# Kernel tuning notes

Measured on AMD Instinct MI355X. Metric: run time of the kernel, lower is better.

## Reference

```python
import jax, jax.numpy as jnp
import numpy as np

N_NODES = 100000
N_EDGES = 1600000
IN_DIM = 64
HID_DIM = 64
OUT_DIM = 1


def setup_inputs() -> dict:
    key = jax.random.key(0)
    ks = jax.random.split(key, 5)
    x = jax.random.normal(ks[0], (N_NODES, IN_DIM), dtype=jnp.float32)
    edge_index = jax.random.randint(ks[1], (2, N_EDGES), 0, N_NODES, dtype=jnp.int64)
    s1 = 1.0 / np.sqrt(IN_DIM)
    s2 = 1.0 / np.sqrt(HID_DIM)
    W1 = jax.random.normal(ks[2], (IN_DIM, HID_DIM), dtype=jnp.float32) * s1
    b1 = jnp.zeros((HID_DIM,), dtype=jnp.float32)
    W2 = jax.random.normal(ks[3], (HID_DIM, HID_DIM), dtype=jnp.float32) * s2
    b2 = jnp.zeros((HID_DIM,), dtype=jnp.float32)
    Wp = jax.random.normal(ks[4], (HID_DIM, OUT_DIM), dtype=jnp.float32) * s2
    bp = jnp.zeros((OUT_DIM,), dtype=jnp.float32)
    return {"x": x, "edge_index": edge_index, "W1": W1, "b1": b1,
            "W2": W2, "b2": b2, "Wp": Wp, "bp": bp}


def _gcn_conv(x, src, dst, deg_inv_sqrt, W, b):
    # PyG GCNConv: linear transform, then deg-normalized scatter-add aggregation
    h = x @ W  # [N, out]
    norm = deg_inv_sqrt[src] * deg_inv_sqrt[dst]  # [E_total]
    msg = h[src] * norm[:, None]  # gather + scale, [E_total, out]
    agg = jax.ops.segment_sum(msg, dst, num_segments=x.shape[0])
    return agg + b


def reference(x, edge_index, W1, b1, W2, b2, Wp, bp):
    n = x.shape[0]
    # add self-loops (as PyG GCNConv does by default)
    loop = jnp.arange(n, dtype=edge_index.dtype)
    src = jnp.concatenate([edge_index[0], loop])
    dst = jnp.concatenate([edge_index[1], loop])
    # symmetric normalization from in-degree over dst (includes self-loops)
    deg = jax.ops.segment_sum(jnp.ones_like(dst, dtype=x.dtype), dst, num_segments=n)
    deg_inv_sqrt = jnp.where(deg > 0, jax.lax.rsqrt(jnp.maximum(deg, 1e-12)), 0.0)
    h = jax.nn.relu(_gcn_conv(x, src, dst, deg_inv_sqrt, W1, b1))
    # dropout(p=0.3) is identity at eval time
    h = jax.nn.relu(_gcn_conv(h, src, dst, deg_inv_sqrt, W2, b2))
    return h @ Wp + bp  # [N, OUT_DIM]
```

## Files before the change

kernel.cpp:

```cpp
#include <hip/hip_runtime.h>
#include <hip/hip_fp16.h>


#define GNN_N 100000
#define GNN_E 1600000
#define NBUCK 391
#define HBLK  500
#define EPBH  3200
#define NBLK  250
#define EPB   6400
#define SCTILE 16
#define STAGE_CAP 4864
#define DUMMY_OFF (GNN_N * 128)

typedef _Float16 half8 __attribute__((ext_vector_type(8)));
typedef float f32x4 __attribute__((ext_vector_type(4)));

__global__ __launch_bounds__(256) void k_hist(const int* __restrict__ dst,
                                              int* __restrict__ hist,
                                              __half* __restrict__ TA,
                                              __half* __restrict__ TB) {
    __shared__ int h[NBUCK];
    for (int i = threadIdx.x; i < NBUCK; i += 256) h[i] = 0;
    if (blockIdx.x == 0 && threadIdx.x < 16) {
        uint4 z = {0, 0, 0, 0};
        int t = threadIdx.x;
        __half* base = (t < 8) ? TA : TB;
        *(uint4*)((char*)base + DUMMY_OFF + (t & 7) * 16) = z;
    }
    __syncthreads();
    int b = blockIdx.x;
    int e0 = b * EPBH, e1 = min(e0 + EPBH, GNN_E);
    for (int e = e0 + threadIdx.x * 4; e < e1; e += 1024) {
        int4 d = *(const int4*)(dst + e);
        atomicAdd(&h[d.x >> 8], 1);
        atomicAdd(&h[d.y >> 8], 1);
        atomicAdd(&h[d.z >> 8], 1);
        atomicAdd(&h[d.w >> 8], 1);
    }
    __syncthreads();
    for (int i = threadIdx.x; i < NBUCK; i += 256)
        hist[b * NBUCK + i] = h[i];
}

__global__ __launch_bounds__(256) void k_cscan(int* __restrict__ hist,
                                               int* __restrict__ tot) {
    __shared__ int tile[256][SCTILE + 1];
    int k0 = blockIdx.x * SCTILE;
    int b = threadIdx.x;
    int lane = b & 63, w = b >> 6;
    int cSub = lane >> 4;
    int l16 = lane & 15;
    int col = w * 4 + cSub;
    int run = 0;
    for (int pass = 0; pass < 2; ++pass) {
        int r = pass * 256 + b;
#pragma unroll
        for (int i = 0; i < SCTILE; ++i) {
            int k = k0 + i;
            tile[b][i] = (k < NBUCK && r < HBLK) ? hist[r * NBUCK + k] : 0;
        }
        __syncthreads();
        for (int chunk = 0; chunk < 16; ++chunk) {
            int idx = chunk * 16 + l16;
            int v = tile[idx][col];
            int s = v;
#pragma unroll
            for (int o = 1; o < 16; o <<= 1) {
                int t = __shfl_up(s, o);
                if (l16 >= o) s += t;
            }
            tile[idx][col] = s - v + run;
            run += __shfl(s, lane | 15);
        }
        __syncthreads();
#pragma unroll
        for (int i = 0; i < SCTILE; ++i) {
            int k = k0 + i;
            if (k < NBUCK && r < HBLK) hist[r * NBUCK + k] = tile[b][i];
        }
        __syncthreads();
    }
    if (l16 == 0 && k0 + col < NBUCK) tot[k0 + col] = run;
}

__global__ __launch_bounds__(512) void k_btot(const int* __restrict__ tot,
                                              int* __restrict__ bbase,
                                              int* __restrict__ cbase) {
    __shared__ int s[512];
    int t = threadIdx.x;
    int own = (t < NBUCK) ? tot[t] : 0;
    s[t] = own;
    __syncthreads();
    for (int off = 1; off < 512; off <<= 1) {
        int v = (t >= off) ? s[t - off] : 0;
        __syncthreads();
        s[t] += v;
        __syncthreads();
    }
    if (t < NBUCK) {
        int ex = s[t] - own;
        bbase[t] = ex;
        cbase[t] = (ex & ~3) + t * 772;
    }
    if (t == 0) bbase[NBUCK] = GNN_E;
}

__global__ __launch_bounds__(256) void k_part(const int* __restrict__ src,
                                              const int* __restrict__ dst,
                                              const int* __restrict__ hist,
                                              const int* __restrict__ bbase,
                                              unsigned int* __restrict__ part) {
    __shared__ int off[NBUCK];
    int b = blockIdx.x;
    for (int i = threadIdx.x; i < NBUCK; i += 256)
        off[i] = bbase[i] + hist[(2 * b) * NBUCK + i];
    __syncthreads();
    int e0 = b * EPB, e1 = min(e0 + EPB, GNN_E);
    for (int e = e0 + threadIdx.x * 4; e < e1; e += 1024) {
        int4 d = *(const int4*)(dst + e);
        int4 s = *(const int4*)(src + e);
        int sl0 = atomicAdd(&off[d.x >> 8], 1);
        part[sl0] = ((unsigned int)(d.x & 255) << 17) | (unsigned int)s.x;
        int sl1 = atomicAdd(&off[d.y >> 8], 1);
        part[sl1] = ((unsigned int)(d.y & 255) << 17) | (unsigned int)s.y;
        int sl2 = atomicAdd(&off[d.z >> 8], 1);
        part[sl2] = ((unsigned int)(d.z & 255) << 17) | (unsigned int)s.z;
        int sl3 = atomicAdd(&off[d.w >> 8], 1);
        part[sl3] = ((unsigned int)(d.w & 255) << 17) | (unsigned int)s.w;
    }
}

__global__ __launch_bounds__(256) void k_bsort(const unsigned int* __restrict__ part,
                                               const int* __restrict__ bbase,
                                               const int* __restrict__ cbase,
                                               int* __restrict__ csr,
                                               int* __restrict__ rowptr,
                                               int* __restrict__ deg,
                                               float* __restrict__ dis) {
    __shared__ int cnt[256];
    __shared__ int pstart[256];
    __shared__ int bump[256];
    __shared__ int wtot[4];
    __shared__ unsigned int stage[STAGE_CAP];
    int k = blockIdx.x;
    int t = threadIdx.x;
    cnt[t] = 0;
    __syncthreads();
    int e0 = bbase[k], e1 = bbase[k + 1];
    int m = e1 - e0;
    bool fits = (m <= STAGE_CAP);
    for (int i = t; i < m; i += 256) {
        unsigned int p = part[e0 + i];
        if (fits) stage[i] = p;
        atomicAdd(&cnt[p >> 17], 1);
    }
    __syncthreads();
    int c = cnt[t];
    int padded = (c + 3) & ~3;
    int v = padded;
#pragma unroll
    for (int o = 1; o < 64; o <<= 1) {
        int u = __shfl_up(v, o);
        if ((t & 63) >= o) v += u;
    }
    if ((t & 63) == 63) wtot[t >> 6] = v;
    __syncthreads();
    int wb = 0;
#pragma unroll
    for (int j = 0; j < 4; ++j)
        if (j < (t >> 6)) wb += wtot[j];
    pstart[t] = wb + v - padded;
    bump[t] = pstart[t];
    __syncthreads();
    int cb = cbase[k];
    int node = k * 256 + t;
    if (node < GNN_N) {
        rowptr[node] = cb + pstart[t];
        deg[node]    = padded;
        dis[node]    = rsqrtf((float)c + 1.0f);
    }
    for (int i = t; i < m; i += 256) {
        unsigned int p = fits ? stage[i] : part[e0 + i];
        int slot = atomicAdd(&bump[p >> 17], 1);
        csr[cb + slot] = (int)(p & 0x1FFFF) << 7;
    }
    __syncthreads();
    if (node < GNN_N) {
        for (int i = c; i < padded; ++i)
            csr[cb + pstart[t] + i] = DUMMY_OFF;
    }
}

template<typename TIN>
__global__ __launch_bounds__(256) void k_mmf(const TIN* __restrict__ X,
                                             const float* __restrict__ W,
                                             const float* __restrict__ dis,
                                             __half* __restrict__ Y, int n) {
    __shared__ __align__(16) __half Xs[64][72];
    __shared__ __align__(16) __half Wt[64][72];
    __shared__ float disS[64];
    int tid = threadIdx.x;
    int base = blockIdx.x * 64;
    for (int i = tid; i < 4096; i += 256) {
        int k = i >> 6, j = i & 63;
        Wt[j][k] = __float2half(W[i]);
    }
    if (tid < 64) disS[tid] = (base + tid < n) ? dis[base + tid] : 0.f;
    if constexpr (sizeof(TIN) == 4) {
#pragma unroll
        for (int ii = 0; ii < 4; ++ii) {
            int i = ii * 256 + tid;
            int r = i >> 4, c4 = i & 15;
            int row = base + r;
            float4 vv = (row < n) ? ((const float4*)(X + (size_t)row * 64))[c4]
                                  : make_float4(0.f, 0.f, 0.f, 0.f);
            *(__half2*)&Xs[r][c4 * 4 + 0] = __floats2half2_rn(vv.x, vv.y);
            *(__half2*)&Xs[r][c4 * 4 + 2] = __floats2half2_rn(vv.z, vv.w);
        }
    } else {
#pragma unroll
        for (int ii = 0; ii < 2; ++ii) {
            int i = ii * 256 + tid;
            int r = i >> 3, c8 = i & 7;
            int row = base + r;
            uint4 u = {0, 0, 0, 0};
            if (row < n)
                u = *(const uint4*)((const __half*)X + (size_t)row * 64 + c8 * 8);
            *(uint4*)&Xs[r][c8 * 8] = u;
        }
    }
    __syncthreads();
    int w = tid >> 6, lane = tid & 63;
    int ar = w * 16 + (lane & 15);
    int ak = (lane >> 4) * 8;
    half8 a0 = *(const half8*)&Xs[ar][ak];
    half8 a1 = *(const half8*)&Xs[ar][32 + ak];
    f32x4 acc0 = {0.f, 0.f, 0.f, 0.f}, acc1 = acc0, acc2 = acc0, acc3 = acc0;
#define MMCOL(ACC, C) {                                                   \
        half8 b0 = *(const half8*)&Wt[(C) * 16 + (lane & 15)][ak];        \
        half8 b1 = *(const half8*)&Wt[(C) * 16 + (lane & 15)][32 + ak];   \
        ACC = __builtin_amdgcn_mfma_f32_16x16x32_f16(a0, b0, ACC, 0, 0, 0); \
        ACC = __builtin_amdgcn_mfma_f32_16x16x32_f16(a1, b1, ACC, 0, 0, 0); }
    MMCOL(acc0, 0) MMCOL(acc1, 1) MMCOL(acc2, 2) MMCOL(acc3, 3)
#undef MMCOL
    __syncthreads();
#define DST(ACC, C) {                                                     \
        _Pragma("unroll")                                                 \
        for (int i = 0; i < 4; ++i) {                                     \
            int rl = w * 16 + (lane >> 4) * 4 + i;                        \
            Xs[rl][(C) * 16 + (lane & 15)] = __float2half(ACC[i] * disS[rl]); \
        } }
    DST(acc0, 0) DST(acc1, 1) DST(acc2, 2) DST(acc3, 3)
#undef DST
    __syncthreads();
#pragma unroll
    for (int ii = 0; ii < 2; ++ii) {
        int i = ii * 256 + tid;
        int r = i >> 3, c8 = i & 7;
        int row = base + r;
        if (row < n)
            *(uint4*)(Y + (size_t)row * 64 + c8 * 8) = *(const uint4*)&Xs[r][c8 * 8];
    }
}

#define ACC8(A, U) {                                                     \
    float2 f_;                                                           \
    f_ = __half22float2(*(__half2*)&U.x); A[0] += f_.x; A[1] += f_.y;    \
    f_ = __half22float2(*(__half2*)&U.y); A[2] += f_.x; A[3] += f_.y;    \
    f_ = __half22float2(*(__half2*)&U.z); A[4] += f_.x; A[5] += f_.y;    \
    f_ = __half22float2(*(__half2*)&U.w); A[6] += f_.x; A[7] += f_.y; }

template<bool HEAD>
__global__ __launch_bounds__(256) void k_gatherg(
        const __half* __restrict__ T, const int* __restrict__ csr,
        const int* __restrict__ rowptr, const int* __restrict__ deg,
        const float* __restrict__ dis, const float* __restrict__ bias,
        const float* __restrict__ Wp, const float* __restrict__ bp,
        void* __restrict__ outv, int n) {
    int tid = threadIdx.x;
    int q = tid & 7;
    int node = blockIdx.x * 32 + (tid >> 3);
    if (node >= n) return;
    int base = rowptr[node];
    int cnt  = deg[node];
    float dd = dis[node];
    const char* Tq = (const char*)T + q * 16;
    float a0[8], a1[8];
#pragma unroll
    for (int i = 0; i < 8; ++i) { a0[i] = 0.f; a1[i] = 0.f; }
    int j = 0;
    for (; j + 8 <= cnt; j += 8) {
        int4 c0 = *(const int4*)(csr + base + j);
        int4 c1 = *(const int4*)(csr + base + j + 4);
        uint4 u0 = *(const uint4*)(Tq + (size_t)(unsigned)c0.x);
        uint4 u1 = *(const uint4*)(Tq + (size_t)(unsigned)c0.y);
        uint4 u2 = *(const uint4*)(Tq + (size_t)(unsigned)c0.z);
        uint4 u3 = *(const uint4*)(Tq + (size_t)(unsigned)c0.w);
        uint4 u4 = *(const uint4*)(Tq + (size_t)(unsigned)c1.x);
        uint4 u5 = *(const uint4*)(Tq + (size_t)(unsigned)c1.y);
        uint4 u6 = *(const uint4*)(Tq + (size_t)(unsigned)c1.z);
        uint4 u7 = *(const uint4*)(Tq + (size_t)(unsigned)c1.w);
        ACC8(a0, u0) ACC8(a1, u1) ACC8(a0, u2) ACC8(a1, u3)
        ACC8(a0, u4) ACC8(a1, u5) ACC8(a0, u6) ACC8(a1, u7)
    }
    if (j < cnt) {
        int4 c0 = *(const int4*)(csr + base + j);
        uint4 u0 = *(const uint4*)(Tq + (size_t)(unsigned)c0.x);
        uint4 u1 = *(const uint4*)(Tq + (size_t)(unsigned)c0.y);
        uint4 u2 = *(const uint4*)(Tq + (size_t)(unsigned)c0.z);
        uint4 u3 = *(const uint4*)(Tq + (size_t)(unsigned)c0.w);
        ACC8(a0, u0) ACC8(a1, u1) ACC8(a0, u2) ACC8(a1, u3)
    }
    uint4 us = *(const uint4*)(Tq + (size_t)node * 128);
    ACC8(a1, us)
    float4 bb0 = ((const float4*)bias)[q * 2 + 0];
    float4 bb1 = ((const float4*)bias)[q * 2 + 1];
    float r[8];
    r[0] = fmaxf(dd * (a0[0] + a1[0]) + bb0.x, 0.f);
    r[1] = fmaxf(dd * (a0[1] + a1[1]) + bb0.y, 0.f);
    r[2] = fmaxf(dd * (a0[2] + a1[2]) + bb0.z, 0.f);
    r[3] = fmaxf(dd * (a0[3] + a1[3]) + bb0.w, 0.f);
    r[4] = fmaxf(dd * (a0[4] + a1[4]) + bb1.x, 0.f);
    r[5] = fmaxf(dd * (a0[5] + a1[5]) + bb1.y, 0.f);
    r[6] = fmaxf(dd * (a0[6] + a1[6]) + bb1.z, 0.f);
    r[7] = fmaxf(dd * (a0[7] + a1[7]) + bb1.w, 0.f);
    if constexpr (HEAD) {
        float4 w0 = ((const float4*)Wp)[q * 2 + 0];
        float4 w1 = ((const float4*)Wp)[q * 2 + 1];
        float s = r[0] * w0.x + r[1] * w0.y + r[2] * w0.z + r[3] * w0.w
                + r[4] * w1.x + r[5] * w1.y + r[6] * w1.z + r[7] * w1.w;
#pragma unroll
        for (int m = 1; m <= 4; m <<= 1) s += __shfl_xor(s, m);
        if (q == 0) ((float*)outv)[node] = s + bp[0];
    } else {
        __half* op = (__half*)outv + (size_t)node * 64 + q * 8;
        uint4 u;
        *(__half2*)&u.x = __floats2half2_rn(r[0], r[1]);
        *(__half2*)&u.y = __floats2half2_rn(r[2], r[3]);
        *(__half2*)&u.z = __floats2half2_rn(r[4], r[5]);
        *(__half2*)&u.w = __floats2half2_rn(r[6], r[7]);
        *(uint4*)op = u;
    }
}

extern "C" void kernel_launch(void* const* d_in, const int* in_sizes, int n_in,
                              void* d_out, int out_size, void* d_ws, size_t ws_size,
                              hipStream_t stream) {
    const float* x  = (const float*)d_in[0];
    const int*   ei = (const int*)d_in[1];
    const float* W1 = (const float*)d_in[2];
    const float* b1 = (const float*)d_in[3];
    const float* W2 = (const float*)d_in[4];
    const float* b2 = (const float*)d_in[5];
    const float* Wp = (const float*)d_in[6];
    const float* bp = (const float*)d_in[7];
    float* out = (float*)d_out;

    const int N = GNN_N, E = GNN_E;
    const int* srcv = ei;
    const int* dstv = ei + E;

    char* ws = (char*)d_ws;
    int*    hist   = (int*)(ws + 0);
    int*    bbase  = (int*)(ws + 784000);
    int*    cbase  = (int*)(ws + 785600);
    int*    rowptr = (int*)(ws + 787200);
    int*    deg    = (int*)(ws + 1187200);
    float*  dis    = (float*)(ws + 1587200);
    int*    tot    = (int*)(ws + 1587200);
    int*    csr    = (int*)(ws + 1987200);
    __half* TA     = (__half*)(ws + 9597440);
    __half* h1h    = (__half*)(ws + 22410368);
    __half* TB     = (__half*)(ws + 35210368);
    unsigned int* part = (unsigned int*)(ws + 48023296);

    k_hist <<<HBLK, 256, 0, stream>>>(dstv, hist, TA, TB);
    k_cscan<<<(NBUCK + SCTILE - 1) / SCTILE, 256, 0, stream>>>(hist, tot);
    k_btot <<<1, 512, 0, stream>>>(tot, bbase, cbase);
    k_part <<<NBLK, 256, 0, stream>>>(srcv, dstv, hist, bbase, part);
    k_bsort<<<NBUCK, 256, 0, stream>>>(part, bbase, cbase, csr, rowptr, deg, dis);

    k_mmf<float><<<(N + 63) / 64, 256, 0, stream>>>(x, W1, dis, TA, N);
    k_gatherg<false><<<(N + 31) / 32, 256, 0, stream>>>(TA, csr, rowptr, deg, dis,
                                                        b1, nullptr, nullptr, h1h, N);
    k_mmf<__half><<<(N + 63) / 64, 256, 0, stream>>>(h1h, W2, dis, TB, N);
    k_gatherg<true><<<(N + 31) / 32, 256, 0, stream>>>(TB, csr, rowptr, deg, dis,
                                                       b2, Wp, bp, out, N);
}
```

Baseline: 132.0 us.

## Fuse layer-1 aggregation with layer-2 linear transform via in-block MFMA

The first-layer gather kernel now stages its 32 aggregated, ReLU'd rows in shared memory and multiplies them by W2 with MFMA, scaling by deg_inv_sqrt and writing the layer-2 transformed features directly. This removes a separate matmul launch and the write-then-read round trip of the intermediate hidden tensor through global memory. In exchange, each gather block converts W2 into shared memory, uses more LDS and adds barriers, which may lower occupancy of the latency-bound gather. The launch assumes N is divisible by 32.

After: 127.5 us. 1.04x faster.

```diff
diff --git a/kernel.cpp b/kernel.cpp
--- a/kernel.cpp
+++ b/kernel.cpp
@@ -192,8 +192,7 @@
     }
 }
 
-template<typename TIN>
-__global__ __launch_bounds__(256) void k_mmf(const TIN* __restrict__ X,
+__global__ __launch_bounds__(256) void k_mmf(const float* __restrict__ X,
                                              const float* __restrict__ W,
                                              const float* __restrict__ dis,
                                              __half* __restrict__ Y, int n) {
@@ -207,28 +206,15 @@
         Wt[j][k] = __float2half(W[i]);
     }
     if (tid < 64) disS[tid] = (base + tid < n) ? dis[base + tid] : 0.f;
-    if constexpr (sizeof(TIN) == 4) {
-#pragma unroll
-        for (int ii = 0; ii < 4; ++ii) {
-            int i = ii * 256 + tid;
-            int r = i >> 4, c4 = i & 15;
-            int row = base + r;
-            float4 vv = (row < n) ? ((const float4*)(X + (size_t)row * 64))[c4]
-                                  : make_float4(0.f, 0.f, 0.f, 0.f);
-            *(__half2*)&Xs[r][c4 * 4 + 0] = __floats2half2_rn(vv.x, vv.y);
-            *(__half2*)&Xs[r][c4 * 4 + 2] = __floats2half2_rn(vv.z, vv.w);
-        }
-    } else {
-#pragma unroll
-        for (int ii = 0; ii < 2; ++ii) {
-            int i = ii * 256 + tid;
-            int r = i >> 3, c8 = i & 7;
-            int row = base + r;
-            uint4 u = {0, 0, 0, 0};
-            if (row < n)
-                u = *(const uint4*)((const __half*)X + (size_t)row * 64 + c8 * 8);
-            *(uint4*)&Xs[r][c8 * 8] = u;
-        }
+#pragma unroll
+    for (int ii = 0; ii < 4; ++ii) {
+        int i = ii * 256 + tid;
+        int r = i >> 4, c4 = i & 15;
+        int row = base + r;
+        float4 vv = (row < n) ? ((const float4*)(X + (size_t)row * 64))[c4]
+                              : make_float4(0.f, 0.f, 0.f, 0.f);
+        *(__half2*)&Xs[r][c4 * 4 + 0] = __floats2half2_rn(vv.x, vv.y);
+        *(__half2*)&Xs[r][c4 * 4 + 2] = __floats2half2_rn(vv.z, vv.w);
     }
     __syncthreads();
     int w = tid >> 6, lane = tid & 63;
@@ -271,20 +257,26 @@
     f_ = __half22float2(*(__half2*)&U.z); A[4] += f_.x; A[5] += f_.y;    \
     f_ = __half22float2(*(__half2*)&U.w); A[6] += f_.x; A[7] += f_.y; }
 
-template<bool HEAD>
-__global__ __launch_bounds__(256) void k_gatherg(
+__global__ __launch_bounds__(256) void k_gatherW2(
         const __half* __restrict__ T, const int* __restrict__ csr,
         const int* __restrict__ rowptr, const int* __restrict__ deg,
         const float* __restrict__ dis, const float* __restrict__ bias,
-        const float* __restrict__ Wp, const float* __restrict__ bp,
-        void* __restrict__ outv, int n) {
+        const float* __restrict__ W2, __half* __restrict__ TB) {
+    __shared__ __align__(16) __half Wt[64][72];
+    __shared__ __align__(16) __half Rt[32][72];
+    __shared__ float disT[32];
     int tid = threadIdx.x;
+    for (int i = tid; i < 4096; i += 256) {
+        int k = i >> 6, j = i & 63;
+        Wt[j][k] = __float2half(W2[i]);
+    }
     int q = tid & 7;
-    int node = blockIdx.x * 32 + (tid >> 3);
-    if (node >= n) return;
+    int nl = tid >> 3;
+    int node = blockIdx.x * 32 + nl;
     int base = rowptr[node];
     int cnt  = deg[node];
     float dd = dis[node];
+    if (q == 0) disT[nl] = dd;
     const char* Tq = (const char*)T + q * 16;
     float a0[8], a1[8];
 #pragma unroll
@@ -325,23 +317,107 @@
     r[5] = fmaxf(dd * (a0[5] + a1[5]) + bb1.y, 0.f);
     r[6] = fmaxf(dd * (a0[6] + a1[6]) + bb1.z, 0.f);
     r[7] = fmaxf(dd * (a0[7] + a1[7]) + bb1.w, 0.f);
-    if constexpr (HEAD) {
-        float4 w0 = ((const float4*)Wp)[q * 2 + 0];
-        float4 w1 = ((const float4*)Wp)[q * 2 + 1];
-        float s = r[0] * w0.x + r[1] * w0.y + r[2] * w0.z + r[3] * w0.w
-                + r[4] * w1.x + r[5] * w1.y + r[6] * w1.z + r[7] * w1.w;
-#pragma unroll
-        for (int m = 1; m <= 4; m <<= 1) s += __shfl_xor(s, m);
-        if (q == 0) ((float*)outv)[node] = s + bp[0];
-    } else {
-        __half* op = (__half*)outv + (size_t)node * 64 + q * 8;
-        uint4 u;
-        *(__half2*)&u.x = __floats2half2_rn(r[0], r[1]);
-        *(__half2*)&u.y = __floats2half2_rn(r[2], r[3]);
-        *(__half2*)&u.z = __floats2half2_rn(r[4], r[5]);
-        *(__half2*)&u.w = __floats2half2_rn(r[6], r[7]);
-        *(uint4*)op = u;
-    }
+    uint4 u;
+    *(__half2*)&u.x = __floats2half2_rn(r[0], r[1]);
+    *(__half2*)&u.y = __floats2half2_rn(r[2], r[3]);
+    *(__half2*)&u.z = __floats2half2_rn(r[4], r[5]);
+    *(__half2*)&u.w = __floats2half2_rn(r[6], r[7]);
+    *(uint4*)&Rt[nl][q * 8] = u;
+    __syncthreads();
+    int w = tid >> 6, lane = tid & 63;
+    int band = w >> 1, cg = w & 1;
+    int ar = band * 16 + (lane & 15);
+    int ak = (lane >> 4) * 8;
+    half8 fa0 = *(const half8*)&Rt[ar][ak];
+    half8 fa1 = *(const half8*)&Rt[ar][32 + ak];
+    f32x4 acc0 = {0.f, 0.f, 0.f, 0.f}, acc1 = acc0;
+    {
+        int c0 = cg * 2, c1 = cg * 2 + 1;
+        half8 b00 = *(const half8*)&Wt[c0 * 16 + (lane & 15)][ak];
+        half8 b01 = *(const half8*)&Wt[c0 * 16 + (lane & 15)][32 + ak];
+        half8 b10 = *(const half8*)&Wt[c1 * 16 + (lane & 15)][ak];
+        half8 b11 = *(const half8*)&Wt[c1 * 16 + (lane & 15)][32 + ak];
+        acc0 = __builtin_amdgcn_mfma_f32_16x16x32_f16(fa0, b00, acc0, 0, 0, 0);
+        acc0 = __builtin_amdgcn_mfma_f32_16x16x32_f16(fa1, b01, acc0, 0, 0, 0);
+        acc1 = __builtin_amdgcn_mfma_f32_16x16x32_f16(fa0, b10, acc1, 0, 0, 0);
+        acc1 = __builtin_amdgcn_mfma_f32_16x16x32_f16(fa1, b11, acc1, 0, 0, 0);
+    }
+    __syncthreads();
+#pragma unroll
+    for (int i = 0; i < 4; ++i) {
+        int rl = band * 16 + (lane >> 4) * 4 + i;
+        float dsc = disT[rl];
+        Rt[rl][(cg * 2 + 0) * 16 + (lane & 15)] = __float2half(acc0[i] * dsc);
+        Rt[rl][(cg * 2 + 1) * 16 + (lane & 15)] = __float2half(acc1[i] * dsc);
+    }
+    __syncthreads();
+    {
+        int r8 = tid >> 3, c8 = tid & 7;
+        int row = blockIdx.x * 32 + r8;
+        *(uint4*)(TB + (size_t)row * 64 + c8 * 8) = *(const uint4*)&Rt[r8][c8 * 8];
+    }
+}
+
+__global__ __launch_bounds__(256) void k_gatherg(
+        const __half* __restrict__ T, const int* __restrict__ csr,
+        const int* __restrict__ rowptr, const int* __restrict__ deg,
+        const float* __restrict__ dis, const float* __restrict__ bias,
+        const float* __restrict__ Wp, const float* __restrict__ bp,
+        float* __restrict__ out, int n) {
+    int tid = threadIdx.x;
+    int q = tid & 7;
+    int node = blockIdx.x * 32 + (tid >> 3);
+    if (node >= n) return;
+    int base = rowptr[node];
+    int cnt  = deg[node];
+    float dd = dis[node];
+    const char* Tq = (const char*)T + q * 16;
+    float a0[8], a1[8];
+#pragma unroll
+    for (int i = 0; i < 8; ++i) { a0[i] = 0.f; a1[i] = 0.f; }
+    int j = 0;
+    for (; j + 8 <= cnt; j += 8) {
+        int4 c0 = *(const int4*)(csr + base + j);
+        int4 c1 = *(const int4*)(csr + base + j + 4);
+        uint4 u0 = *(const uint4*)(Tq + (size_t)(unsigned)c0.x);
+        uint4 u1 = *(const uint4*)(Tq + (size_t)(unsigned)c0.y);
+        uint4 u2 = *(const uint4*)(Tq + (size_t)(unsigned)c0.z);
+        uint4 u3 = *(const uint4*)(Tq + (size_t)(unsigned)c0.w);
+        uint4 u4 = *(const uint4*)(Tq + (size_t)(unsigned)c1.x);
+        uint4 u5 = *(const uint4*)(Tq + (size_t)(unsigned)c1.y);
+        uint4 u6 = *(const uint4*)(Tq + (size_t)(unsigned)c1.z);
+        uint4 u7 = *(const uint4*)(Tq + (size_t)(unsigned)c1.w);
+        ACC8(a0, u0) ACC8(a1, u1) ACC8(a0, u2) ACC8(a1, u3)
+        ACC8(a0, u4) ACC8(a1, u5) ACC8(a0, u6) ACC8(a1, u7)
+    }
+    if (j < cnt) {
+        int4 c0 = *(const int4*)(csr + base + j);
+        uint4 u0 = *(const uint4*)(Tq + (size_t)(unsigned)c0.x);
+        uint4 u1 = *(const uint4*)(Tq + (size_t)(unsigned)c0.y);
+        uint4 u2 = *(const uint4*)(Tq + (size_t)(unsigned)c0.z);
+        uint4 u3 = *(const uint4*)(Tq + (size_t)(unsigned)c0.w);
+        ACC8(a0, u0) ACC8(a1, u1) ACC8(a0, u2) ACC8(a1, u3)
+    }
+    uint4 us = *(const uint4*)(Tq + (size_t)node * 128);
+    ACC8(a1, us)
+    float4 bb0 = ((const float4*)bias)[q * 2 + 0];
+    float4 bb1 = ((const float4*)bias)[q * 2 + 1];
+    float r[8];
+    r[0] = fmaxf(dd * (a0[0] + a1[0]) + bb0.x, 0.f);
+    r[1] = fmaxf(dd * (a0[1] + a1[1]) + bb0.y, 0.f);
+    r[2] = fmaxf(dd * (a0[2] + a1[2]) + bb0.z, 0.f);
+    r[3] = fmaxf(dd * (a0[3] + a1[3]) + bb0.w, 0.f);
+    r[4] = fmaxf(dd * (a0[4] + a1[4]) + bb1.x, 0.f);
+    r[5] = fmaxf(dd * (a0[5] + a1[5]) + bb1.y, 0.f);
+    r[6] = fmaxf(dd * (a0[6] + a1[6]) + bb1.z, 0.f);
+    r[7] = fmaxf(dd * (a0[7] + a1[7]) + bb1.w, 0.f);
+    float4 w0 = ((const float4*)Wp)[q * 2 + 0];
+    float4 w1 = ((const float4*)Wp)[q * 2 + 1];
+    float s = r[0] * w0.x + r[1] * w0.y + r[2] * w0.z + r[3] * w0.w
+            + r[4] * w1.x + r[5] * w1.y + r[6] * w1.z + r[7] * w1.w;
+#pragma unroll
+    for (int m = 1; m <= 4; m <<= 1) s += __shfl_xor(s, m);
+    if (q == 0) out[node] = s + bp[0];
 }
 
 extern "C" void kernel_launch(void* const* d_in, const int* in_sizes, int n_in,
@@ -371,9 +447,8 @@
     int*    tot    = (int*)(ws + 1587200);
     int*    csr    = (int*)(ws + 1987200);
     __half* TA     = (__half*)(ws + 9597440);
-    __half* h1h    = (__half*)(ws + 22410368);
-    __half* TB     = (__half*)(ws + 35210368);
-    unsigned int* part = (unsigned int*)(ws + 48023296);
+    __half* TB     = (__half*)(ws + 22400000);
+    unsigned int* part = (unsigned int*)(ws + 35200256);
 
     k_hist <<<HBLK, 256, 0, stream>>>(dstv, hist, TA, TB);
     k_cscan<<<(NBUCK + SCTILE - 1) / SCTILE, 256, 0, stream>>>(hist, tot);
@@ -381,10 +456,8 @@
     k_part <<<NBLK, 256, 0, stream>>>(srcv, dstv, hist, bbase, part);
     k_bsort<<<NBUCK, 256, 0, stream>>>(part, bbase, cbase, csr, rowptr, deg, dis);
 
-    k_mmf<float><<<(N + 63) / 64, 256, 0, stream>>>(x, W1, dis, TA, N);
-    k_gatherg<false><<<(N + 31) / 32, 256, 0, stream>>>(TA, csr, rowptr, deg, dis,
-                                                        b1, nullptr, nullptr, h1h, N);
-    k_mmf<__half><<<(N + 63) / 64, 256, 0, stream>>>(h1h, W2, dis, TB, N);
-    k_gatherg<true><<<(N + 31) / 32, 256, 0, stream>>>(TB, csr, rowptr, deg, dis,
-                                                       b2, Wp, bp, out, N);
-}
+    k_mmf<<<(N + 63) / 64, 256, 0, stream>>>(x, W1, dis, TA, N);
+    k_gatherW2<<<N / 32, 256, 0, stream>>>(TA, csr, rowptr, deg, dis, b1, W2, TB);
+    k_gatherg<<<(N + 31) / 32, 256, 0, stream>>>(TB, csr, rowptr, deg, dis,
+                                                 b2, Wp, bp, out, N);
+}
```
